# Kernel optimization log

Hardware: AMD Instinct MI355X
Metric: run time of the kernel (lower is better)

## Reference

```python
import jax, jax.numpy as jnp
import numpy as np

EPS = 1e-7  # K.epsilon()
NUM_ROUTING = 3


def squash(v, axis=-1):
    s2 = jnp.sum(v * v, axis=axis, keepdims=True)
    return (s2 / (1.0 + s2) / jnp.sqrt(s2 + EPS)) * v


def setup_inputs() -> dict:
    key = jax.random.key(0)
    k1, k2 = jax.random.split(key)
    # [B, H, W, in_caps, in_dim]
    x = jax.random.normal(k1, (32, 16, 16, 16, 8), dtype=jnp.float32)
    # W: [input_num_capsule=H*W*in_caps, num_capsule, in_dim, dim_vector]
    W = jax.random.normal(k2, (4096, 10, 8, 16), dtype=jnp.float32) * 0.05
    return {"x": x, "W": W}


def reference(x, W):
    B = x.shape[0]
    N = x.shape[1] * x.shape[2] * x.shape[3]  # input_num_capsule
    C = W.shape[1]                            # num_capsule
    u = x.reshape(B, N, x.shape[4])           # [B, N, Din]
    # inputs_hat[b,n,c,d] = sum_i u[b,n,i] * W[n,c,i,d]  (tf.scan batch_dot)
    u_hat = jnp.einsum('bni,ncid->bncd', u, W)            # [B, N, C, D]
    u_hat_stop = jax.lax.stop_gradient(u_hat)

    # routing logits (bias), starts shared across batch: [1, N, C]
    b = jnp.zeros((1, N, C), dtype=x.dtype)
    v = None
    for i in range(NUM_ROUTING):
        c = jax.nn.softmax(b, axis=2)                     # softmax over capsules
        uh = u_hat if i == NUM_ROUTING - 1 else u_hat_stop
        v = squash(jnp.sum(c[..., None] * uh, axis=1, keepdims=True))  # [B,1,C,D]
        if i < NUM_ROUTING - 1:
            # bias update uses non-stopped inputs_hat (as in original)
            b = b + jnp.sum(u_hat * v, axis=-1)           # [B, N, C]
    return v.reshape(-1, C, W.shape[3])                   # [B, C, D]
```

## Files before the change

### kernel.cpp

```cpp
#include <hip/hip_runtime.h>
#include <hip/hip_bf16.h>


#define BB 32
#define NN 4096
#define CC 10
#define DIN 8
#define DD 16
#define NCHUNK 8
#define NCHUNKS_TOTAL (NN / NCHUNK)
#define TPB 512
#define SOUT (BB * CC * DD)
#define UHATF ((size_t)BB * NN * CC * DD)

template<int CTRL>
__device__ __forceinline__ float dpp_mov(float x) {
    return __int_as_float(__builtin_amdgcn_update_dpp(
        0, __float_as_int(x), CTRL, 0xF, 0xF, true));
}
__device__ __forceinline__ float row_sum16(float x) {
    x += dpp_mov<0xB1>(x);
    x += dpp_mov<0x4E>(x);
    x += dpp_mov<0x124>(x);
    x += dpp_mov<0x128>(x);
    return x;
}

__global__ __launch_bounds__(TPB) void caps_uhat_pass0(
    const float* __restrict__ xg,
    const float* __restrict__ Wg,
    float* __restrict__ uhat,
    float* __restrict__ part)
{
    __shared__ float Wl[NCHUNK * CC * DIN * DD];

    const int t    = threadIdx.x;
    const int lane = t & 63;
    const int bqu  = __builtin_amdgcn_readfirstlane(t >> 6);
    const int cq   = lane >> 4;
    const int d    = lane & 15;

    float acc[4][3];
    #pragma unroll
    for (int bb = 0; bb < 4; ++bb)
        #pragma unroll
        for (int r = 0; r < 3; ++r) acc[bb][r] = 0.f;

    for (int chunk = blockIdx.x; chunk < NCHUNKS_TOTAL; chunk += gridDim.x) {
        const int n0 = chunk * NCHUNK;

        {
            const float4* WgV = (const float4*)Wg;
            #pragma unroll
            for (int wi = 0; wi < 5; ++wi) {
                int m4 = t + wi * TPB;
                int j  = m4 / 320;
                int q  = m4 - j * 320;
                int c  = q >> 5, i = (q & 31) >> 2, d0 = (q & 3) << 2;
                float4 v = WgV[(size_t)n0 * 320 + m4];
                const float* vf = (const float*)&v;
                float* plane = Wl + j * 1280;
                int h = i >> 2, wd = i & 3;
                #pragma unroll
                for (int k = 0; k < 4; ++k) {
                    int R = c * DD + d0 + k;
                    int U = (R * 2 + h) ^ ((R >> 2) & 7);
                    plane[U * 4 + wd] = vf[k];
                }
            }
        }
        __syncthreads();

        #pragma unroll 1
        for (int j = 0; j < NCHUNK; ++j) {
            const float4* planeV = (const float4*)(Wl + j * 1280);
            const int n = n0 + j;

            float ub[4][8];
            #pragma unroll
            for (int bb = 0; bb < 4; ++bb) {
                const float* up = xg + ((size_t)(bqu * 4 + bb) * NN + n) * DIN;
                #pragma unroll
                for (int i = 0; i < 8; ++i) ub[bb][i] = up[i];
            }

            #pragma unroll
            for (int r = 0; r < 3; ++r) {
                int c = cq + 4 * r;
                float w0=0,w1=0,w2=0,w3=0,w4=0,w5=0,w6=0,w7=0;
                if (c < CC) {
                    int R  = c * DD + d;
                    int sw = (R >> 2) & 7;
                    float4 a0 = planeV[(R * 2) ^ sw];
                    float4 a1 = planeV[(R * 2 + 1) ^ sw];
                    w0=a0.x; w1=a0.y; w2=a0.z; w3=a0.w;
                    w4=a1.x; w5=a1.y; w6=a1.z; w7=a1.w;
                }
                #pragma unroll
                for (int bb = 0; bb < 4; ++bb) {
                    int b = bqu * 4 + bb;
                    float s = 0.f;
                    s = fmaf(ub[bb][0], w0, s); s = fmaf(ub[bb][1], w1, s);
                    s = fmaf(ub[bb][2], w2, s); s = fmaf(ub[bb][3], w3, s);
                    s = fmaf(ub[bb][4], w4, s); s = fmaf(ub[bb][5], w5, s);
                    s = fmaf(ub[bb][6], w6, s); s = fmaf(ub[bb][7], w7, s);
                    if (c < CC)
                        uhat[((size_t)b * NN + n) * (CC * DD) + lane + 64 * r] = s;
                    acc[bb][r] += s;
                }
            }
        }
        __syncthreads();
    }

    float* dst = part + (size_t)blockIdx.x * SOUT;
    #pragma unroll
    for (int bb = 0; bb < 4; ++bb) {
        int b = bqu * 4 + bb;
        #pragma unroll
        for (int r = 0; r < 3; ++r) {
            int c = cq + 4 * r;
            if (c < CC) dst[(b * CC + c) * DD + d] = acc[bb][r] * (1.0f / CC);
        }
    }
}

__global__ __launch_bounds__(TPB) void caps_routed(
    const float* __restrict__ uhat,
    const float* __restrict__ vprev,
    float* __restrict__ part)
{
    const int t    = threadIdx.x;
    const int lane = t & 63;
    const int bqu  = __builtin_amdgcn_readfirstlane(t >> 6);
    const int cq   = lane >> 4;
    const int d    = lane & 15;

    float vv[4][3];
    #pragma unroll
    for (int bb = 0; bb < 4; ++bb) {
        int b = bqu * 4 + bb;
        #pragma unroll
        for (int r = 0; r < 3; ++r) {
            int c = cq + 4 * r;
            vv[bb][r] = (c < CC) ? vprev[(b * CC + c) * DD + d] : 0.f;
        }
    }

    float acc[4][3];
    #pragma unroll
    for (int bb = 0; bb < 4; ++bb)
        #pragma unroll
        for (int r = 0; r < 3; ++r) acc[bb][r] = 0.f;

    for (int chunk = blockIdx.x; chunk < NCHUNKS_TOTAL; chunk += gridDim.x) {
        const int n0 = chunk * NCHUNK;
        #pragma unroll 1
        for (int j = 0; j < NCHUNK; ++j) {
            const int n = n0 + j;
            float uh[4][3];
            #pragma unroll
            for (int bb = 0; bb < 4; ++bb) {
                const float* base =
                    uhat + ((size_t)(bqu * 4 + bb) * NN + n) * (CC * DD);
                #pragma unroll
                for (int r = 0; r < 3; ++r) {
                    int c = cq + 4 * r;
                    uh[bb][r] = (c < CC) ? base[lane + 64 * r] : 0.f;
                }
            }
            #pragma unroll
            for (int bb = 0; bb < 4; ++bb) {
                float dot0 = row_sum16(uh[bb][0] * vv[bb][0]);
                float dot1 = row_sum16(uh[bb][1] * vv[bb][1]);
                float dot2 = row_sum16(uh[bb][2] * vv[bb][2]);
                float e0 = __expf(dot0);
                float e1 = __expf(dot1);
                float e2 = (cq < 2) ? __expf(dot2) : 0.f;
                float den = e0 + e1 + e2;
                den += __shfl_xor(den, 16, 64);
                den += __shfl_xor(den, 32, 64);
                float inv = __builtin_amdgcn_rcpf(den);
                acc[bb][0] = fmaf(e0 * inv, uh[bb][0], acc[bb][0]);
                acc[bb][1] = fmaf(e1 * inv, uh[bb][1], acc[bb][1]);
                acc[bb][2] = fmaf(e2 * inv, uh[bb][2], acc[bb][2]);
            }
        }
    }

    float* dst = part + (size_t)blockIdx.x * SOUT;
    #pragma unroll
    for (int bb = 0; bb < 4; ++bb) {
        int b = bqu * 4 + bb;
        #pragma unroll
        for (int r = 0; r < 3; ++r) {
            int c = cq + 4 * r;
            if (c < CC) dst[(b * CC + c) * DD + d] = acc[bb][r];
        }
    }
}

template<int UNIFORM, int PARTIALS>
__global__ __launch_bounds__(TPB) void caps_pass(
    const float* __restrict__ xg,
    const float* __restrict__ Wg,
    const float* __restrict__ vprev,
    float* __restrict__ outp)
{
    __shared__ float Wl[NCHUNK * CC * DIN * DD];

    const int t    = threadIdx.x;
    const int lane = t & 63;
    const int bqu  = __builtin_amdgcn_readfirstlane(t >> 6);
    const int cq   = lane >> 4;
    const int d    = lane & 15;

    float vv[4][3];
    if (!UNIFORM) {
        #pragma unroll
        for (int bb = 0; bb < 4; ++bb) {
            int b = bqu * 4 + bb;
            #pragma unroll
            for (int r = 0; r < 3; ++r) {
                int c = cq + 4 * r;
                vv[bb][r] = (c < CC) ? vprev[(b * CC + c) * DD + d] : 0.f;
            }
        }
    }

    float acc[4][3];
    #pragma unroll
    for (int bb = 0; bb < 4; ++bb)
        #pragma unroll
        for (int r = 0; r < 3; ++r) acc[bb][r] = 0.f;

    for (int chunk = blockIdx.x; chunk < NCHUNKS_TOTAL; chunk += gridDim.x) {
        const int n0 = chunk * NCHUNK;
        {
            const float4* WgV = (const float4*)Wg;
            #pragma unroll
            for (int wi = 0; wi < 5; ++wi) {
                int m4 = t + wi * TPB;
                int j = m4 / 320, q = m4 - j * 320;
                int c = q >> 5, i = (q & 31) >> 2, d0 = (q & 3) << 2;
                float4 v = WgV[(size_t)n0 * 320 + m4];
                const float* vf = (const float*)&v;
                float* plane = Wl + j * 1280;
                int h = i >> 2, wd = i & 3;
                #pragma unroll
                for (int k = 0; k < 4; ++k) {
                    int R = c * DD + d0 + k;
                    int U = (R * 2 + h) ^ ((R >> 2) & 7);
                    plane[U * 4 + wd] = vf[k];
                }
            }
        }
        __syncthreads();

        #pragma unroll 1
        for (int j = 0; j < NCHUNK; ++j) {
            const float4* planeV = (const float4*)(Wl + j * 1280);
            float ub[4][8];
            #pragma unroll
            for (int bb = 0; bb < 4; ++bb) {
                const float* up = xg + ((size_t)(bqu * 4 + bb) * NN + n0 + j) * DIN;
                #pragma unroll
                for (int i = 0; i < 8; ++i) ub[bb][i] = up[i];
            }
            float uh[4][3];
            #pragma unroll
            for (int r = 0; r < 3; ++r) {
                int c = cq + 4 * r;
                float w0=0,w1=0,w2=0,w3=0,w4=0,w5=0,w6=0,w7=0;
                if (c < CC) {
                    int R = c * DD + d, sw = (R >> 2) & 7;
                    float4 a0 = planeV[(R * 2) ^ sw];
                    float4 a1 = planeV[(R * 2 + 1) ^ sw];
                    w0=a0.x; w1=a0.y; w2=a0.z; w3=a0.w;
                    w4=a1.x; w5=a1.y; w6=a1.z; w7=a1.w;
                }
                #pragma unroll
                for (int bb = 0; bb < 4; ++bb) {
                    float s = 0.f;
                    s = fmaf(ub[bb][0], w0, s); s = fmaf(ub[bb][1], w1, s);
                    s = fmaf(ub[bb][2], w2, s); s = fmaf(ub[bb][3], w3, s);
                    s = fmaf(ub[bb][4], w4, s); s = fmaf(ub[bb][5], w5, s);
                    s = fmaf(ub[bb][6], w6, s); s = fmaf(ub[bb][7], w7, s);
                    uh[bb][r] = s;
                }
            }
            #pragma unroll
            for (int bb = 0; bb < 4; ++bb) {
                float w0, w1, w2;
                if (UNIFORM) { w0 = w1 = w2 = 1.0f / CC; }
                else {
                    float dot0 = row_sum16(uh[bb][0] * vv[bb][0]);
                    float dot1 = row_sum16(uh[bb][1] * vv[bb][1]);
                    float dot2 = row_sum16(uh[bb][2] * vv[bb][2]);
                    float e0 = __expf(dot0), e1 = __expf(dot1);
                    float e2 = (cq < 2) ? __expf(dot2) : 0.f;
                    float den = e0 + e1 + e2;
                    den += __shfl_xor(den, 16, 64);
                    den += __shfl_xor(den, 32, 64);
                    float inv = __builtin_amdgcn_rcpf(den);
                    w0 = e0 * inv; w1 = e1 * inv; w2 = e2 * inv;
                }
                acc[bb][0] = fmaf(w0, uh[bb][0], acc[bb][0]);
                acc[bb][1] = fmaf(w1, uh[bb][1], acc[bb][1]);
                acc[bb][2] = fmaf(w2, uh[bb][2], acc[bb][2]);
            }
        }
        __syncthreads();
    }

    #pragma unroll
    for (int bb = 0; bb < 4; ++bb) {
        int b = bqu * 4 + bb;
        #pragma unroll
        for (int r = 0; r < 3; ++r) {
            int c = cq + 4 * r;
            if (c < CC) {
                if (PARTIALS) (outp + (size_t)blockIdx.x * SOUT)[(b * CC + c) * DD + d] = acc[bb][r];
                else atomicAdd(&outp[(b * CC + c) * DD + d], acc[bb][r]);
            }
        }
    }
}

template<int MODE>
__global__ __launch_bounds__(256) void caps_reduce(
    const float* __restrict__ part, int G,
    float* __restrict__ vsum, float* __restrict__ outF)
{
    __shared__ float red[256];
    const int row = blockIdx.x;
    const int t = threadIdx.x;
    const int d = t & 15, ks = t >> 4;
    const int per = G >> 4;
    const float* p = part + row * DD + d;
    float s = 0.f;
    for (int kk = 0; kk < per; ++kk)
        s += p[(size_t)(ks * per + kk) * SOUT];
    red[t] = s;
    __syncthreads();
    if (t < 16) {
        float sd = 0.f;
        #pragma unroll
        for (int k2 = 0; k2 < 16; ++k2) sd += red[k2 * 16 + t];
        float s2 = sd * sd;
        #pragma unroll
        for (int m = 1; m < 16; m <<= 1) s2 += __shfl_xor(s2, m, 64);
        float f = s2 / ((1.f + s2) * sqrtf(s2 + 1e-7f));
        float v = f * sd;
        int idx = row * DD + t;
        if (MODE == 0) vsum[idx] = v;
        if (MODE == 1) vsum[idx] += v;
        if (MODE == 2) outF[idx] = v;
    }
}

template<int MODE>
__global__ __launch_bounds__(512) void caps_squash(
    const float* __restrict__ sIn, float* __restrict__ vsum,
    float* __restrict__ outF)
{
    int r = blockIdx.x * blockDim.x + threadIdx.x;
    if (r >= BB * CC) return;
    const float* p = sIn + (size_t)r * DD;
    float sv[DD]; float s2 = 0.f;
    #pragma unroll
    for (int d = 0; d < DD; ++d) { sv[d] = p[d]; s2 = fmaf(sv[d], sv[d], s2); }
    float f = s2 / ((1.f + s2) * sqrtf(s2 + 1e-7f));
    #pragma unroll
    for (int d = 0; d < DD; ++d) {
        float v = f * sv[d];
        int idx = r * DD + d;
        if (MODE == 0) vsum[idx] = v;
        if (MODE == 1) vsum[idx] += v;
        if (MODE == 2) outF[idx] = v;
    }
}

extern "C" void kernel_launch(void* const* d_in, const int* in_sizes, int n_in,
                              void* d_out, int out_size, void* d_ws, size_t ws_size,
                              hipStream_t stream) {
    const float* x; const float* Wt;
    if (in_sizes[0] == BB * NN * DIN) { x = (const float*)d_in[0]; Wt = (const float*)d_in[1]; }
    else                              { Wt = (const float*)d_in[0]; x = (const float*)d_in[1]; }
    float* out = (float*)d_out;
    float* ws = (float*)d_ws;

    const int G = 512;
    const size_t need = (UHATF + (size_t)(G + 1) * SOUT) * sizeof(float);

    if (ws_size >= need) {
        float* uhat = ws;
        float* part = ws + UHATF;
        float* vsum = part + (size_t)G * SOUT;
        caps_uhat_pass0<<<G, TPB, 0, stream>>>(x, Wt, uhat, part);
        caps_reduce<0><<<BB*CC, 256, 0, stream>>>(part, G, vsum, nullptr);
        caps_routed<<<G, TPB, 0, stream>>>(uhat, vsum, part);
        caps_reduce<1><<<BB*CC, 256, 0, stream>>>(part, G, vsum, nullptr);
        caps_routed<<<G, TPB, 0, stream>>>(uhat, vsum, part);
        caps_reduce<2><<<BB*CC, 256, 0, stream>>>(part, G, vsum, out);
    } else {
        const size_t wsf = ws_size / sizeof(float);
        int Gf = 0;
        const int cands[5] = {512, 256, 128, 64, 32};
        for (int ci = 0; ci < 5; ++ci)
            if (wsf >= (size_t)(cands[ci] + 1) * SOUT) { Gf = cands[ci]; break; }
        if (Gf > 0) {
            float* part = ws;
            float* vsum = ws + (size_t)Gf * SOUT;
            caps_pass<1,1><<<Gf, TPB, 0, stream>>>(x, Wt, nullptr, part);
            caps_reduce<0><<<BB*CC, 256, 0, stream>>>(part, Gf, vsum, nullptr);
            caps_pass<0,1><<<Gf, TPB, 0, stream>>>(x, Wt, vsum, part);
            caps_reduce<1><<<BB*CC, 256, 0, stream>>>(part, Gf, vsum, nullptr);
            caps_pass<0,1><<<Gf, TPB, 0, stream>>>(x, Wt, vsum, part);
            caps_reduce<2><<<BB*CC, 256, 0, stream>>>(part, Gf, vsum, out);
        } else {
            float* sAcc = ws;
            float* vsum = ws + SOUT;
            hipMemsetAsync(sAcc, 0, SOUT * sizeof(float), stream);
            caps_pass<1,0><<<64, TPB, 0, stream>>>(x, Wt, nullptr, sAcc);
            caps_squash<0><<<1, 512, 0, stream>>>(sAcc, vsum, nullptr);
            hipMemsetAsync(sAcc, 0, SOUT * sizeof(float), stream);
            caps_pass<0,0><<<64, TPB, 0, stream>>>(x, Wt, vsum, sAcc);
            caps_squash<1><<<1, 512, 0, stream>>>(sAcc, vsum, nullptr);
            hipMemsetAsync(sAcc, 0, SOUT * sizeof(float), stream);
            caps_pass<0,0><<<64, TPB, 0, stream>>>(x, Wt, vsum, sAcc);
            caps_squash<2><<<1, 512, 0, stream>>>(sAcc, nullptr, out);
        }
    }
}
```

Baseline: 91.59 us.

## Store u_hat intermediate in bf16 and load W directly from global

The materialized u_hat buffer, written once and read twice by the routing passes, is now stored as bfloat16 instead of fp32, halving its memory traffic. The pass-0 kernel also drops the LDS staging of W with its swizzled layout and sync barriers, reading W straight from global with strided loads. Each block now handles exactly one chunk, with no grid-stride loop. This adds bf16 rounding error to the routing inputs and may make W loads less coalesced.

```diff
diff --git a/kernel.cpp b/kernel.cpp
--- a/kernel.cpp
+++ b/kernel.cpp
@@ -11,7 +11,7 @@
 #define NCHUNKS_TOTAL (NN / NCHUNK)
 #define TPB 512
 #define SOUT (BB * CC * DD)
-#define UHATF ((size_t)BB * NN * CC * DD)
+#define UHATE ((size_t)BB * NN * CC * DD)
 
 template<int CTRL>
 __device__ __forceinline__ float dpp_mov(float x) {
@@ -26,14 +26,16 @@
     return x;
 }
 
+__device__ __forceinline__ float bf2f(unsigned short u) {
+    return __uint_as_float((unsigned int)u << 16);
+}
+
 __global__ __launch_bounds__(TPB) void caps_uhat_pass0(
     const float* __restrict__ xg,
     const float* __restrict__ Wg,
-    float* __restrict__ uhat,
+    __hip_bfloat16* __restrict__ uhat,
     float* __restrict__ part)
 {
-    __shared__ float Wl[NCHUNK * CC * DIN * DD];
-
     const int t    = threadIdx.x;
     const int lane = t & 63;
     const int bqu  = __builtin_amdgcn_readfirstlane(t >> 6);
@@ -46,71 +48,44 @@
         #pragma unroll
         for (int r = 0; r < 3; ++r) acc[bb][r] = 0.f;
 
-    for (int chunk = blockIdx.x; chunk < NCHUNKS_TOTAL; chunk += gridDim.x) {
-        const int n0 = chunk * NCHUNK;
-
-        {
-            const float4* WgV = (const float4*)Wg;
-            #pragma unroll
-            for (int wi = 0; wi < 5; ++wi) {
-                int m4 = t + wi * TPB;
-                int j  = m4 / 320;
-                int q  = m4 - j * 320;
-                int c  = q >> 5, i = (q & 31) >> 2, d0 = (q & 3) << 2;
-                float4 v = WgV[(size_t)n0 * 320 + m4];
-                const float* vf = (const float*)&v;
-                float* plane = Wl + j * 1280;
-                int h = i >> 2, wd = i & 3;
-                #pragma unroll
-                for (int k = 0; k < 4; ++k) {
-                    int R = c * DD + d0 + k;
-                    int U = (R * 2 + h) ^ ((R >> 2) & 7);
-                    plane[U * 4 + wd] = vf[k];
-                }
-            }
-        }
-        __syncthreads();
-
-        #pragma unroll 1
-        for (int j = 0; j < NCHUNK; ++j) {
-            const float4* planeV = (const float4*)(Wl + j * 1280);
-            const int n = n0 + j;
-
-            float ub[4][8];
+    const int n0 = blockIdx.x * NCHUNK;
+
+    #pragma unroll 1
+    for (int j = 0; j < NCHUNK; ++j) {
+        const int n = n0 + j;
+
+        float ub[4][8];
+        #pragma unroll
+        for (int bb = 0; bb < 4; ++bb) {
+            const float* up = xg + ((size_t)(bqu * 4 + bb) * NN + n) * DIN;
+            #pragma unroll
+            for (int i = 0; i < 8; ++i) ub[bb][i] = up[i];
+        }
+
+        #pragma unroll
+        for (int r = 0; r < 3; ++r) {
+            const int c = cq + 4 * r;
+            float wf[8];
+            if (c < CC) {
+                const float* wp = Wg + (size_t)n * (CC * DIN * DD) + c * (DIN * DD) + d;
+                #pragma unroll
+                for (int i = 0; i < 8; ++i) wf[i] = wp[i * DD];
+            } else {
+                #pragma unroll
+                for (int i = 0; i < 8; ++i) wf[i] = 0.f;
+            }
             #pragma unroll
             for (int bb = 0; bb < 4; ++bb) {
-                const float* up = xg + ((size_t)(bqu * 4 + bb) * NN + n) * DIN;
-                #pragma unroll
-                for (int i = 0; i < 8; ++i) ub[bb][i] = up[i];
-            }
-
-            #pragma unroll
-            for (int r = 0; r < 3; ++r) {
-                int c = cq + 4 * r;
-                float w0=0,w1=0,w2=0,w3=0,w4=0,w5=0,w6=0,w7=0;
-                if (c < CC) {
-                    int R  = c * DD + d;
-                    int sw = (R >> 2) & 7;
-                    float4 a0 = planeV[(R * 2) ^ sw];
-                    float4 a1 = planeV[(R * 2 + 1) ^ sw];
-                    w0=a0.x; w1=a0.y; w2=a0.z; w3=a0.w;
-                    w4=a1.x; w5=a1.y; w6=a1.z; w7=a1.w;
-                }
-                #pragma unroll
-                for (int bb = 0; bb < 4; ++bb) {
-                    int b = bqu * 4 + bb;
-                    float s = 0.f;
-                    s = fmaf(ub[bb][0], w0, s); s = fmaf(ub[bb][1], w1, s);
-                    s = fmaf(ub[bb][2], w2, s); s = fmaf(ub[bb][3], w3, s);
-                    s = fmaf(ub[bb][4], w4, s); s = fmaf(ub[bb][5], w5, s);
-                    s = fmaf(ub[bb][6], w6, s); s = fmaf(ub[bb][7], w7, s);
-                    if (c < CC)
-                        uhat[((size_t)b * NN + n) * (CC * DD) + lane + 64 * r] = s;
-                    acc[bb][r] += s;
-                }
-            }
-        }
-        __syncthreads();
+                const int b = bqu * 4 + bb;
+                float s = 0.f;
+                #pragma unroll
+                for (int i = 0; i < 8; ++i) s = fmaf(ub[bb][i], wf[i], s);
+                if (c < CC)
+                    uhat[((size_t)b * NN + n) * (CC * DD) + lane + 64 * r] =
+                        __float2bfloat16(s);
+                acc[bb][r] += s;
+            }
+        }
     }
 
     float* dst = part + (size_t)blockIdx.x * SOUT;
@@ -126,7 +101,7 @@
 }
 
 __global__ __launch_bounds__(TPB) void caps_routed(
-    const float* __restrict__ uhat,
+    const __hip_bfloat16* __restrict__ uhat,
     const float* __restrict__ vprev,
     float* __restrict__ part)
 {
@@ -153,38 +128,37 @@
         #pragma unroll
         for (int r = 0; r < 3; ++r) acc[bb][r] = 0.f;
 
-    for (int chunk = blockIdx.x; chunk < NCHUNKS_TOTAL; chunk += gridDim.x) {
-        const int n0 = chunk * NCHUNK;
-        #pragma unroll 1
-        for (int j = 0; j < NCHUNK; ++j) {
-            const int n = n0 + j;
-            float uh[4][3];
-            #pragma unroll
-            for (int bb = 0; bb < 4; ++bb) {
-                const float* base =
-                    uhat + ((size_t)(bqu * 4 + bb) * NN + n) * (CC * DD);
-                #pragma unroll
-                for (int r = 0; r < 3; ++r) {
-                    int c = cq + 4 * r;
-                    uh[bb][r] = (c < CC) ? base[lane + 64 * r] : 0.f;
-                }
-            }
-            #pragma unroll
-            for (int bb = 0; bb < 4; ++bb) {
-                float dot0 = row_sum16(uh[bb][0] * vv[bb][0]);
-                float dot1 = row_sum16(uh[bb][1] * vv[bb][1]);
-                float dot2 = row_sum16(uh[bb][2] * vv[bb][2]);
-                float e0 = __expf(dot0);
-                float e1 = __expf(dot1);
-                float e2 = (cq < 2) ? __expf(dot2) : 0.f;
-                float den = e0 + e1 + e2;
-                den += __shfl_xor(den, 16, 64);
-                den += __shfl_xor(den, 32, 64);
-                float inv = __builtin_amdgcn_rcpf(den);
-                acc[bb][0] = fmaf(e0 * inv, uh[bb][0], acc[bb][0]);
-                acc[bb][1] = fmaf(e1 * inv, uh[bb][1], acc[bb][1]);
-                acc[bb][2] = fmaf(e2 * inv, uh[bb][2], acc[bb][2]);
-            }
+    const int n0 = blockIdx.x * NCHUNK;
+
+    #pragma unroll 1
+    for (int j = 0; j < NCHUNK; ++j) {
+        const int n = n0 + j;
+        float uh[4][3];
+        #pragma unroll
+        for (int bb = 0; bb < 4; ++bb) {
+            const __hip_bfloat16* base =
+                uhat + ((size_t)(bqu * 4 + bb) * NN + n) * (CC * DD);
+            #pragma unroll
+            for (int r = 0; r < 3; ++r) {
+                int c = cq + 4 * r;
+                uh[bb][r] = (c < CC) ? __bfloat162float(base[lane + 64 * r]) : 0.f;
+            }
+        }
+        #pragma unroll
+        for (int bb = 0; bb < 4; ++bb) {
+            float dot0 = row_sum16(uh[bb][0] * vv[bb][0]);
+            float dot1 = row_sum16(uh[bb][1] * vv[bb][1]);
+            float dot2 = row_sum16(uh[bb][2] * vv[bb][2]);
+            float e0 = __expf(dot0);
+            float e1 = __expf(dot1);
+            float e2 = (cq < 2) ? __expf(dot2) : 0.f;
+            float den = e0 + e1 + e2;
+            den += __shfl_xor(den, 16, 64);
+            den += __shfl_xor(den, 32, 64);
+            float inv = __builtin_amdgcn_rcpf(den);
+            acc[bb][0] = fmaf(e0 * inv, uh[bb][0], acc[bb][0]);
+            acc[bb][1] = fmaf(e1 * inv, uh[bb][1], acc[bb][1]);
+            acc[bb][2] = fmaf(e2 * inv, uh[bb][2], acc[bb][2]);
         }
     }
 
@@ -391,11 +365,13 @@
     float* ws = (float*)d_ws;
 
     const int G = 512;
-    const size_t need = (UHATF + (size_t)(G + 1) * SOUT) * sizeof(float);
+    const size_t uhat_floats = UHATE / 2;
+    const size_t need = UHATE * sizeof(__hip_bfloat16)
+                      + (size_t)(G + 1) * SOUT * sizeof(float);
 
     if (ws_size >= need) {
-        float* uhat = ws;
-        float* part = ws + UHATF;
+        __hip_bfloat16* uhat = (__hip_bfloat16*)ws;
+        float* part = ws + uhat_floats;
         float* vsum = part + (size_t)G * SOUT;
         caps_uhat_pass0<<<G, TPB, 0, stream>>>(x, Wt, uhat, part);
         caps_reduce<0><<<BB*CC, 256, 0, stream>>>(part, G, vsum, nullptr);
```

After: 93.50 us. +2.1%, slower.
